# Kernel tuning notes

Measured on AMD Instinct MI355X. Metric: run time of the kernel, lower is better.

Reference implementation:

```python
import jax, jax.numpy as jnp
import numpy as np

IN_FEATURES = 8192
OUT_FEATURES = 14336
M_TOKENS = 64


def _dequant_rowwise_int4(w_packed, w_scales):
    # w_packed: [out, in//2], each byte holds two signed int4 values
    # (low nibble = even k index, high nibble = odd k index, two's complement)
    low = w_packed & 0xF
    high = (w_packed >> 4) & 0xF
    q = jnp.stack([low, high], axis=-1).reshape(w_packed.shape[0], -1)  # [out, in]
    q = jnp.where(q >= 8, q - 16, q).astype(jnp.float32)
    return q * w_scales[:, None]  # [out, in]


def setup_inputs() -> dict:
    key = jax.random.key(0)
    k1, k2, k3, k4 = jax.random.split(key, 4)
    x = jax.random.normal(k1, (M_TOKENS, IN_FEATURES), dtype=jnp.float32)
    w_packed = jax.random.randint(k2, (OUT_FEATURES, IN_FEATURES // 2), 0, 256, dtype=jnp.int32)
    # per-row scales, small positive values as produced by max-abs/7 quantization
    w_scales = jax.random.uniform(k3, (OUT_FEATURES,), dtype=jnp.float32) * 0.02 + 1e-4
    bias = jax.random.normal(k4, (OUT_FEATURES,), dtype=jnp.float32)
    return {"x": x, "w_packed": w_packed, "w_scales": w_scales, "bias": bias}


def reference(x, w_packed, w_scales, bias):
    original_shape = x.shape[:-1]
    x_2d = x.reshape(-1, IN_FEATURES)
    w = _dequant_rowwise_int4(w_packed, w_scales)  # [out, in]
    y = x_2d @ w.T + bias[None, :]  # [M, out]
    return y.reshape(*original_shape, OUT_FEATURES)
```

## Files before the change

kernel.cpp:

```cpp
#include <hip/hip_runtime.h>

#define IN_F   8192
#define OUT_F  14336
#define M_TOK  64
#define KPI    4096
#define BN     64
#define NBLK   (OUT_F / BN)
#define KSPLIT 8
#define GPERK  8
#define NG     64
#define PSTR   (M_TOK * OUT_F)

typedef __attribute__((ext_vector_type(8))) short          bf16x8;
typedef __attribute__((ext_vector_type(8))) unsigned short u16x8;
typedef __attribute__((ext_vector_type(4))) float          f32x4;

__device__ __forceinline__ unsigned short f2bf_rne(float f) {
    unsigned u = __builtin_bit_cast(unsigned, f);
    u += 0x7FFFu + ((u >> 16) & 1u);
    return (unsigned short)(u >> 16);
}

__global__ __launch_bounds__(256) void qlin_prep(const float* __restrict__ x,
                                                 unsigned short* __restrict__ xs) {
    int tid  = blockIdx.x * 256 + threadIdx.x;
    int lane = tid & 63;
    int mt   = (tid >> 6) & 3;
    int fg   = tid >> 8;
    int q = lane >> 4, t = lane & 15;
    const float* src = x + (size_t)(mt * 16 + t) * IN_F + fg * 32 + q * 8;
    u16x8 o;
#pragma unroll
    for (int j = 0; j < 8; ++j) o[j] = f2bf_rne(src[j]);
    *reinterpret_cast<u16x8*>(xs + (size_t)tid * 8) = o;
}

__global__ __launch_bounds__(256) void qlin_repack(const int* __restrict__ wp,
                                                   unsigned* __restrict__ rep) {
    int tid = blockIdx.x * 256 + threadIdx.x;
    int n   = tid >> 10;
    int pg  = tid & 1023;
    int4 v = *reinterpret_cast<const int4*>(wp + (size_t)n * KPI + pg * 4);
    unsigned d = (unsigned)(v.x & 255) | ((unsigned)(v.y & 255) << 8)
               | ((unsigned)(v.z & 255) << 16) | ((unsigned)(v.w & 255) << 24);
    int G = n >> 4, t = n & 15;
    int g = pg >> 4, i = (pg & 15) >> 2, q = pg & 3;
    rep[(((size_t)(G * 64 + g) * 64) + q * 16 + t) * 4 + i] = d;
}

__device__ __forceinline__ int unpack2_bf16(int v) {
    int q0 = ((int)((unsigned)v << 28)) >> 28;
    int q1 = ((int)((unsigned)v << 24)) >> 28;
    unsigned u0 = __builtin_bit_cast(unsigned, (float)q0);
    unsigned u1 = __builtin_bit_cast(unsigned, (float)q1);
    return (int)((u0 >> 16) | (u1 & 0xFFFF0000u));
}

__device__ __forceinline__ bf16x8 unpack_frag(unsigned d) {
    int4 pk;
    pk.x = unpack2_bf16((int)(d));
    pk.y = unpack2_bf16((int)(d >> 8));
    pk.z = unpack2_bf16((int)(d >> 16));
    pk.w = unpack2_bf16((int)(d >> 24));
    return __builtin_bit_cast(bf16x8, pk);
}

__global__ __launch_bounds__(256) void qlin_gemm(const unsigned short* __restrict__ xs,
                                                 const unsigned* __restrict__ rep,
                                                 const float* __restrict__ scales,
                                                 float* __restrict__ part) {
    const int tid  = threadIdx.x;
    const int wave = tid >> 6;
    const int lane = tid & 63;
    const int t = lane & 15;
    const int q = lane >> 4;

    const int nblk = blockIdx.x % NBLK;
    const int kblk = blockIdx.x / NBLK;
    const int G    = nblk * 4 + wave;
    const int n    = G * 16 + t;

    const unsigned* wbase = rep + (((size_t)(G * 64 + kblk * GPERK) * 64) + q * 16 + t) * 4;

    f32x4 acc[4] = {};

#pragma unroll
    for (int gi = 0; gi < GPERK; ++gi) {
        uint4 wd = *reinterpret_cast<const uint4*>(wbase + (size_t)gi * 256);
#pragma unroll
        for (int i = 0; i < 4; ++i) {
            const unsigned d = (i == 0) ? wd.x : (i == 1) ? wd.y : (i == 2) ? wd.z : wd.w;
            bf16x8 b = unpack_frag(d);
            const int F = (kblk * GPERK + gi) * 4 + i;
#pragma unroll
            for (int mt = 0; mt < 4; ++mt) {
                bf16x8 a = *reinterpret_cast<const bf16x8*>(
                    xs + ((size_t)(F * 4 + mt) * 64 + lane) * 8);
                acc[mt] = __builtin_amdgcn_mfma_f32_16x16x32_bf16(a, b, acc[mt], 0, 0, 0);
            }
        }
    }

    const float sc = scales[n];
    float* p = part + (size_t)kblk * PSTR;
#pragma unroll
    for (int mt = 0; mt < 4; ++mt)
#pragma unroll
        for (int r = 0; r < 4; ++r)
            p[(size_t)(mt * 16 + q * 4 + r) * OUT_F + n] = acc[mt][r] * sc;
}

__global__ __launch_bounds__(256) void qlin_reduce(const float* __restrict__ part,
                                                   const float* __restrict__ bias,
                                                   float* __restrict__ out) {
    int g = blockIdx.x * 256 + threadIdx.x;
    float4 acc = reinterpret_cast<const float4*>(bias)[g % (OUT_F / 4)];
#pragma unroll
    for (int s = 0; s < KSPLIT; ++s) {
        float4 v = reinterpret_cast<const float4*>(part + (size_t)s * PSTR)[g];
        acc.x += v.x; acc.y += v.y; acc.z += v.z; acc.w += v.w;
    }
    reinterpret_cast<float4*>(out)[g] = acc;
}

extern "C" void kernel_launch(void* const* d_in, const int* in_sizes, int n_in,
                              void* d_out, int out_size, void* d_ws, size_t ws_size,
                              hipStream_t stream) {
    const float* x    = (const float*)d_in[0];
    const int*   wp   = (const int*)d_in[1];
    const float* sc   = (const float*)d_in[2];
    const float* bias = (const float*)d_in[3];
    float* out = (float*)d_out;

    unsigned short* xs   = (unsigned short*)d_ws;
    unsigned*       rp   = (unsigned*)((char*)d_ws + (1 << 20));
    float*          part = (float*)((char*)d_ws + (64u << 20));

    qlin_prep<<<256, 256, 0, stream>>>(x, xs);
    qlin_repack<<<(OUT_F * (KPI / 4)) / 256, 256, 0, stream>>>(wp, rp);
    qlin_gemm<<<NBLK * KSPLIT, 256, 0, stream>>>(xs, rp, sc, part);
    qlin_reduce<<<(M_TOK * OUT_F) / 4 / 256, 256, 0, stream>>>(part, bias, out);
}
```

Baseline: 405.6 us.

## Restructure GEMM split-K with in-block wave reduction and LDS-staged weight repack

The GEMM is reorganised so each block covers 32 output columns, with its four waves splitting the K range and summing their partials in shared memory. That cuts the global split-K partial count from 8 to 4 and shrinks partial-buffer traffic. Each wave now loads two weight fragments and reuses each activation fragment across two MFMAs. The repack kernel stages packed words through LDS so global stores are coalesced 16-byte writes, and the per-row scale moves into the final reduce. The cost is extra LDS use and a barrier in the GEMM, which may limit occupancy.

```diff
diff --git a/kernel.cpp b/kernel.cpp
--- a/kernel.cpp
+++ b/kernel.cpp
@@ -4,11 +4,8 @@
 #define OUT_F  14336
 #define M_TOK  64
 #define KPI    4096
-#define BN     64
-#define NBLK   (OUT_F / BN)
-#define KSPLIT 8
-#define GPERK  8
-#define NG     64
+#define NBLK   448
+#define KSPLIT 4
 #define PSTR   (M_TOK * OUT_F)
 
 typedef __attribute__((ext_vector_type(8))) short          bf16x8;
@@ -37,15 +34,27 @@
 
 __global__ __launch_bounds__(256) void qlin_repack(const int* __restrict__ wp,
                                                    unsigned* __restrict__ rep) {
-    int tid = blockIdx.x * 256 + threadIdx.x;
-    int n   = tid >> 10;
-    int pg  = tid & 1023;
-    int4 v = *reinterpret_cast<const int4*>(wp + (size_t)n * KPI + pg * 4);
-    unsigned d = (unsigned)(v.x & 255) | ((unsigned)(v.y & 255) << 8)
-               | ((unsigned)(v.z & 255) << 16) | ((unsigned)(v.w & 255) << 24);
-    int G = n >> 4, t = n & 15;
-    int g = pg >> 4, i = (pg & 15) >> 2, q = pg & 3;
-    rep[(((size_t)(G * 64 + g) * 64) + q * 16 + t) * 4 + i] = d;
+    __shared__ unsigned lds[2048];
+    const int G   = blockIdx.x >> 3;
+    const int g8  = blockIdx.x & 7;
+    const int tid = threadIdx.x;
+    const int r = tid >> 4, T = tid & 15;
+    const int q = T & 3, i = T >> 2;
+    const int* src = wp + (size_t)(G * 16 + r) * KPI + T * 4;
+#pragma unroll
+    for (int j = 0; j < 8; ++j) {
+        const int g = g8 * 8 + j;
+        int4 v = *reinterpret_cast<const int4*>(src + 64 * g);
+        unsigned d = (unsigned)(v.x & 255) | ((unsigned)(v.y & 255) << 8)
+                   | ((unsigned)(v.z & 255) << 16) | ((unsigned)(v.w & 255) << 24);
+        lds[j * 256 + q * 64 + r * 4 + i] = d;
+    }
+    __syncthreads();
+    unsigned* dst = rep + ((size_t)G * 64 + g8 * 8) * 256;
+#pragma unroll
+    for (int s = 0; s < 2; ++s)
+        *reinterpret_cast<uint4*>(dst + s * 1024 + tid * 4) =
+            *reinterpret_cast<const uint4*>(&lds[s * 1024 + tid * 4]);
 }
 
 __device__ __forceinline__ int unpack2_bf16(int v) {
@@ -65,62 +74,90 @@
     return __builtin_bit_cast(bf16x8, pk);
 }
 
-__global__ __launch_bounds__(256) void qlin_gemm(const unsigned short* __restrict__ xs,
-                                                 const unsigned* __restrict__ rep,
-                                                 const float* __restrict__ scales,
-                                                 float* __restrict__ part) {
+__global__ __launch_bounds__(256, 4) void qlin_gemm(const unsigned short* __restrict__ xs,
+                                                    const unsigned* __restrict__ rep,
+                                                    float* __restrict__ part) {
+    __shared__ float red[4 * 2048];
     const int tid  = threadIdx.x;
     const int wave = tid >> 6;
     const int lane = tid & 63;
     const int t = lane & 15;
     const int q = lane >> 4;
 
-    const int nblk = blockIdx.x % NBLK;
+    const int nb   = blockIdx.x % NBLK;
     const int kblk = blockIdx.x / NBLK;
-    const int G    = nblk * 4 + wave;
-    const int n    = G * 16 + t;
+    const int g0   = kblk * 16 + wave * 4;
 
-    const unsigned* wbase = rep + (((size_t)(G * 64 + kblk * GPERK) * 64) + q * 16 + t) * 4;
+    const unsigned* b0p = rep + ((size_t)((nb * 2)     * 64 + g0) * 64 + q * 16 + t) * 4;
+    const unsigned* b1p = rep + ((size_t)((nb * 2 + 1) * 64 + g0) * 64 + q * 16 + t) * 4;
 
-    f32x4 acc[4] = {};
+    f32x4 acc[2][4] = {};
 
 #pragma unroll
-    for (int gi = 0; gi < GPERK; ++gi) {
-        uint4 wd = *reinterpret_cast<const uint4*>(wbase + (size_t)gi * 256);
+    for (int gi = 0; gi < 4; ++gi) {
+        uint4 w0 = *reinterpret_cast<const uint4*>(b0p + (size_t)gi * 256);
+        uint4 w1 = *reinterpret_cast<const uint4*>(b1p + (size_t)gi * 256);
+        const unsigned* d0 = reinterpret_cast<const unsigned*>(&w0);
+        const unsigned* d1 = reinterpret_cast<const unsigned*>(&w1);
 #pragma unroll
         for (int i = 0; i < 4; ++i) {
-            const unsigned d = (i == 0) ? wd.x : (i == 1) ? wd.y : (i == 2) ? wd.z : wd.w;
-            bf16x8 b = unpack_frag(d);
-            const int F = (kblk * GPERK + gi) * 4 + i;
+            bf16x8 b0 = unpack_frag(d0[i]);
+            bf16x8 b1 = unpack_frag(d1[i]);
+            const int F = (g0 + gi) * 4 + i;
 #pragma unroll
             for (int mt = 0; mt < 4; ++mt) {
                 bf16x8 a = *reinterpret_cast<const bf16x8*>(
                     xs + ((size_t)(F * 4 + mt) * 64 + lane) * 8);
-                acc[mt] = __builtin_amdgcn_mfma_f32_16x16x32_bf16(a, b, acc[mt], 0, 0, 0);
+                acc[0][mt] = __builtin_amdgcn_mfma_f32_16x16x32_bf16(a, b0, acc[0][mt], 0, 0, 0);
+                acc[1][mt] = __builtin_amdgcn_mfma_f32_16x16x32_bf16(a, b1, acc[1][mt], 0, 0, 0);
             }
         }
     }
 
-    const float sc = scales[n];
-    float* p = part + (size_t)kblk * PSTR;
 #pragma unroll
-    for (int mt = 0; mt < 4; ++mt)
+    for (int ng = 0; ng < 2; ++ng)
 #pragma unroll
-        for (int r = 0; r < 4; ++r)
-            p[(size_t)(mt * 16 + q * 4 + r) * OUT_F + n] = acc[mt][r] * sc;
+        for (int mt = 0; mt < 4; ++mt)
+#pragma unroll
+            for (int r = 0; r < 4; ++r)
+                red[wave * 2048 + (mt * 16 + q * 4 + r) * 32 + ng * 16 + t] = acc[ng][mt][r];
+    __syncthreads();
+
+    const int m  = tid >> 2;
+    const int nq = tid & 3;
+    float* p = part + (size_t)kblk * PSTR + (size_t)m * OUT_F + nb * 32 + nq * 8;
+    float4 v0, v1;
+#pragma unroll
+    for (int e = 0; e < 4; ++e) {
+        const int a0 = m * 32 + nq * 8 + e;
+        const int a1 = a0 + 4;
+        v0[e] = red[a0] + red[2048 + a0] + red[4096 + a0] + red[6144 + a0];
+        v1[e] = red[a1] + red[2048 + a1] + red[4096 + a1] + red[6144 + a1];
+    }
+    *reinterpret_cast<float4*>(p)     = v0;
+    *reinterpret_cast<float4*>(p + 4) = v1;
 }
 
 __global__ __launch_bounds__(256) void qlin_reduce(const float* __restrict__ part,
+                                                   const float* __restrict__ scales,
                                                    const float* __restrict__ bias,
                                                    float* __restrict__ out) {
-    int g = blockIdx.x * 256 + threadIdx.x;
-    float4 acc = reinterpret_cast<const float4*>(bias)[g % (OUT_F / 4)];
+    int g  = blockIdx.x * 256 + threadIdx.x;
+    int n4 = g % (OUT_F / 4);
+    float4 s4 = reinterpret_cast<const float4*>(scales)[n4];
+    float4 b4 = reinterpret_cast<const float4*>(bias)[n4];
+    float4 a = {0.f, 0.f, 0.f, 0.f};
 #pragma unroll
     for (int s = 0; s < KSPLIT; ++s) {
-        float4 v = reinterpret_cast<const float4*>(part + (size_t)s * PSTR)[g];
-        acc.x += v.x; acc.y += v.y; acc.z += v.z; acc.w += v.w;
+        float4 v = reinterpret_cast<const float4*>(part)[(size_t)s * (PSTR / 4) + g];
+        a.x += v.x; a.y += v.y; a.z += v.z; a.w += v.w;
     }
-    reinterpret_cast<float4*>(out)[g] = acc;
+    float4 o;
+    o.x = a.x * s4.x + b4.x;
+    o.y = a.y * s4.y + b4.y;
+    o.z = a.z * s4.z + b4.z;
+    o.w = a.w * s4.w + b4.w;
+    reinterpret_cast<float4*>(out)[g] = o;
 }
 
 extern "C" void kernel_launch(void* const* d_in, const int* in_sizes, int n_in,
@@ -137,7 +174,7 @@
     float*          part = (float*)((char*)d_ws + (64u << 20));
 
     qlin_prep<<<256, 256, 0, stream>>>(x, xs);
-    qlin_repack<<<(OUT_F * (KPI / 4)) / 256, 256, 0, stream>>>(wp, rp);
-    qlin_gemm<<<NBLK * KSPLIT, 256, 0, stream>>>(xs, rp, sc, part);
-    qlin_reduce<<<(M_TOK * OUT_F) / 4 / 256, 256, 0, stream>>>(part, bias, out);
+    qlin_repack<<<896 * 8, 256, 0, stream>>>(wp, rp);
+    qlin_gemm<<<NBLK * KSPLIT, 256, 0, stream>>>(xs, rp, part);
+    qlin_reduce<<<(M_TOK * OUT_F) / 4 / 256, 256, 0, stream>>>(part, sc, bias, out);
 }
```

Result: faster. 370.7 us (-8.6%).
